# Kernel tuning notes

Measured on AMD Instinct MI355X. Metric: run time of the kernel, lower is better.

## Reference

```python
import jax, jax.numpy as jnp
import numpy as np

DIM = 192
HEADS = 4
EPS = 1e-12  # F.normalize default eps


def setup_inputs() -> dict:
    key = jax.random.key(0)
    k0, k1, k2, k3 = jax.random.split(key, 4)
    x = jax.random.normal(k0, (4, DIM, 128, 128), dtype=jnp.float32)
    # qkv 1x1 conv weight: [3*dim, dim, 1, 1] -> stored as [3*dim, dim]
    w_qkv = jax.random.normal(k1, (3 * DIM, DIM), dtype=jnp.float32) * (1.0 / np.sqrt(DIM))
    # depthwise 3x3 conv weight: [3*dim, 1, 3, 3]
    w_dw = jax.random.normal(k2, (3 * DIM, 1, 3, 3), dtype=jnp.float32) * (1.0 / 3.0)
    # project_out 1x1 conv weight: [dim, dim]
    w_proj = jax.random.normal(k3, (DIM, DIM), dtype=jnp.float32) * (1.0 / np.sqrt(DIM))
    # temperature: ones(heads,1,1), requires_grad=False in original
    temperature = jnp.ones((HEADS, 1, 1), dtype=jnp.float32)
    return {"x": x, "w_qkv": w_qkv, "w_dw": w_dw, "w_proj": w_proj,
            "temperature": temperature}


def _l2norm(t):
    # F.normalize(t, dim=-1): t / max(||t||_2, eps)
    n = jnp.sqrt(jnp.sum(t * t, axis=-1, keepdims=True))
    return t / jnp.maximum(n, EPS)


def reference(x, w_qkv, w_dw, w_proj, temperature):
    b, c, h, w = x.shape
    ch = c // HEADS  # channels per head
    # 1x1 conv (no bias) == channel GEMM
    qkv = jnp.einsum('oc,bchw->bohw', w_qkv, x)
    # depthwise 3x3 conv, padding=1, groups=3*dim
    qkv = jax.lax.conv_general_dilated(
        qkv, w_dw, window_strides=(1, 1), padding=((1, 1), (1, 1)),
        dimension_numbers=('NCHW', 'OIHW', 'NCHW'),
        feature_group_count=3 * c)
    q, k, v = jnp.split(qkv, 3, axis=1)
    # b (head ch) h w -> b head ch (h w)
    def rearr(t):
        return t.reshape(b, HEADS, ch, h * w)
    q, k, v = rearr(q), rearr(k), rearr(v)
    q = _l2norm(q)
    k = _l2norm(k)
    # channel-channel attention: [b, head, ch, ch]
    attn = jnp.einsum('bhcn,bhdn->bhcd', q, k) * temperature[None]
    attn = jax.nn.softmax(attn, axis=-1)
    out = jnp.einsum('bhcd,bhdn->bhcn', attn, v)
    out = out.reshape(b, c, h, w)
    out = jnp.einsum('oc,bchw->bohw', w_proj, out)
    return out
```

## Files before the change

### kernel.cpp

```cpp
#include <hip/hip_runtime.h>

typedef unsigned short u16;
typedef float f32x4 __attribute__((ext_vector_type(4)));
typedef __bf16 bf16x8 __attribute__((ext_vector_type(8)));
typedef unsigned short u16x8 __attribute__((ext_vector_type(8)));

#define DEV static __device__ __forceinline__

DEV u16 f2bf(float f) {
  unsigned int u = __float_as_uint(f);
  u += 0x7FFFu + ((u >> 16) & 1u);
  return (u16)(u >> 16);
}
DEV float bf2f(u16 h) { return __uint_as_float(((unsigned int)h) << 16); }
DEV u16 to_bf(float f) { return f2bf(f); }
DEV u16 to_bf(u16 h) { return h; }

DEV void gload_lds16(const void* g, void* l) {
  __builtin_amdgcn_global_load_lds(
      (__attribute__((address_space(1))) void*)(unsigned long long)g,
      (__attribute__((address_space(3))) void*)l, 16, 0, 0);
}

__global__ __launch_bounds__(256) void convert_w_kernel(
    const float* __restrict__ in, u16* __restrict__ out, int n) {
  int i = blockIdx.x * 256 + threadIdx.x;
  if (i < n) out[i] = f2bf(in[i]);
}

template <typename TIN>
__global__ __launch_bounds__(256) void transpose_kernel(
    const TIN* __restrict__ in, u16* __restrict__ out,
    size_t inBatch, size_t outBatch, int C) {
  __shared__ u16 ls[64][66];
  const int b = blockIdx.z;
  const int c0 = blockIdx.x * 64, r0 = blockIdx.y * 64;
  const TIN* ip = in + (size_t)b * inBatch;
  u16* op = out + (size_t)b * outBatch;
  const int lane = threadIdx.x & 63, w = threadIdx.x >> 6;
#pragma unroll
  for (int i = 0; i < 16; ++i) {
    const int r = i * 4 + w;
    ls[r][lane] = to_bf(ip[(size_t)(r0 + r) * C + c0 + lane]);
  }
  __syncthreads();
#pragma unroll
  for (int i = 0; i < 16; ++i) {
    const int c = i * 4 + w;
    op[(size_t)(c0 + c) * 192 + r0 + lane] = ls[lane][c];
  }
}

template <bool OUT_BF16>
__global__ __launch_bounds__(256) void gemm_bt_kernel(
    const u16* __restrict__ A, const u16* __restrict__ B, void* __restrict__ Cv,
    size_t aBatch, size_t bBatch, size_t cBatch, int ldC) {
  __shared__ __align__(16) char smem[64 * 129 * 4];
  u16* sA = (u16*)smem;
  u16* sB = (u16*)(smem + 8192);
  float* sC = (float*)smem;

  const int tid = threadIdx.x, wave = tid >> 6, lane = tid & 63;
  const int j0 = blockIdx.x * 64, m0 = blockIdx.y * 128, b = blockIdx.z;
  const u16* Ab = A + (size_t)b * aBatch + (size_t)m0 * 192;
  const u16* Bb = B + (size_t)b * bBatch + (size_t)j0 * 192;
  const int wm = wave & 1, wn = wave >> 1;
  const int l15 = lane & 15, lg = lane >> 4;

  f32x4 acc[4][2];
#pragma unroll
  for (int mi = 0; mi < 4; ++mi)
#pragma unroll
    for (int nj = 0; nj < 2; ++nj) acc[mi][nj] = (f32x4){0.f, 0.f, 0.f, 0.f};

  for (int ks = 0; ks < 6; ++ks) {
    const int k0b = ks * 64;
#pragma unroll
    for (int i = 0; i < 2; ++i) {
      const int flat = (i * 4 + wave) * 1024 + lane * 16;
      const int row = flat >> 6, colb = flat & 63;
      gload_lds16((const char*)Ab + (size_t)row * 384 + k0b + colb,
                  (char*)sA + (i * 4 + wave) * 1024);
    }
    {
      const int flat = wave * 1024 + lane * 16;
      const int row = flat >> 6, colb = flat & 63;
      gload_lds16((const char*)Bb + (size_t)row * 384 + k0b + colb,
                  (char*)sB + wave * 1024);
    }
    asm volatile("s_waitcnt vmcnt(0)" ::: "memory");
    __syncthreads();

    bf16x8 af[4], bfv[2];
#pragma unroll
    for (int mi = 0; mi < 4; ++mi)
      af[mi] = *(const bf16x8*)(sA + ((wm * 64 + mi * 16 + l15) * 32 + lg * 8));
#pragma unroll
    for (int nj = 0; nj < 2; ++nj)
      bfv[nj] = *(const bf16x8*)(sB + ((wn * 32 + nj * 16 + l15) * 32 + lg * 8));
#pragma unroll
    for (int mi = 0; mi < 4; ++mi)
#pragma unroll
      for (int nj = 0; nj < 2; ++nj)
        acc[mi][nj] = __builtin_amdgcn_mfma_f32_16x16x32_bf16(
            af[mi], bfv[nj], acc[mi][nj], 0, 0, 0);
    __syncthreads();
  }

#pragma unroll
  for (int mi = 0; mi < 4; ++mi)
#pragma unroll
    for (int nj = 0; nj < 2; ++nj)
#pragma unroll
      for (int r = 0; r < 4; ++r)
        sC[(wn * 32 + nj * 16 + l15) * 129 + (wm * 64 + mi * 16 + lg * 4 + r)] =
            acc[mi][nj][r];
  __syncthreads();
  if (OUT_BF16) {
    u16* Cb = (u16*)Cv + (size_t)b * cBatch;
#pragma unroll
    for (int i = 0; i < 32; ++i) {
      const int flat = i * 256 + tid;
      const int j = flat >> 7, m = flat & 127;
      Cb[(size_t)(j0 + j) * ldC + m0 + m] = f2bf(sC[j * 129 + m]);
    }
  } else {
    float* Cb = (float*)Cv + (size_t)b * cBatch;
#pragma unroll
    for (int i = 0; i < 32; ++i) {
      const int flat = i * 256 + tid;
      const int j = flat >> 7, m = flat & 127;
      Cb[(size_t)(j0 + j) * ldC + m0 + m] = sC[j * 129 + m];
    }
  }
}

__global__ __launch_bounds__(256) void dwconv_kernel(
    u16* __restrict__ qkv, const float* __restrict__ wdw,
    float* __restrict__ sq) {
  __shared__ u16 img[16384];
  __shared__ float red[4];
  const int o = blockIdx.x, b = blockIdx.y;
  const size_t base = ((size_t)b * 576 + o) * 16384;
  const int tid = threadIdx.x, wave = tid >> 6, lane = tid & 63;
#pragma unroll
  for (int i = 0; i < 8; ++i) {
    const int off = (i * 4 + wave) * 1024;
    gload_lds16((const char*)qkv + base * 2 + off + lane * 16, (char*)img + off);
  }
  asm volatile("s_waitcnt vmcnt(0)" ::: "memory");
  __syncthreads();
  float w[9];
#pragma unroll
  for (int j = 0; j < 9; ++j) w[j] = wdw[o * 9 + j];
  float sqacc = 0.f;
  for (int it = 0; it < 8; ++it) {
    const int chunk = it * 256 + tid;
    const int px0 = chunk * 8;
    const int y = px0 >> 7, x0 = px0 & 127;
    float acc[8];
#pragma unroll
    for (int j = 0; j < 8; ++j) acc[j] = 0.f;
#pragma unroll
    for (int dy = -1; dy <= 1; ++dy) {
      const int yy = y + dy;
      float v[10];
      if (yy >= 0 && yy <= 127) {
        const u16* rowp = img + yy * 128 + x0;
        u16x8 m = *(const u16x8*)rowp;
#pragma unroll
        for (int j = 0; j < 8; ++j) v[j + 1] = bf2f(m[j]);
        v[0] = (x0 > 0) ? bf2f(rowp[-1]) : 0.f;
        v[9] = (x0 < 120) ? bf2f(rowp[8]) : 0.f;
      } else {
#pragma unroll
        for (int j = 0; j < 10; ++j) v[j] = 0.f;
      }
      const float w0 = w[(dy + 1) * 3], w1 = w[(dy + 1) * 3 + 1],
                  w2 = w[(dy + 1) * 3 + 2];
#pragma unroll
      for (int j = 0; j < 8; ++j) acc[j] += w0 * v[j] + w1 * v[j + 1] + w2 * v[j + 2];
    }
    u16x8 ov;
#pragma unroll
    for (int j = 0; j < 8; ++j) {
      sqacc += acc[j] * acc[j];
      ov[j] = f2bf(acc[j]);
    }
    *(u16x8*)(qkv + base + px0) = ov;
  }
#pragma unroll
  for (int s = 32; s > 0; s >>= 1) sqacc += __shfl_xor(sqacc, s, 64);
  if (lane == 0) red[wave] = sqacc;
  __syncthreads();
  if (tid == 0) sq[b * 576 + o] = red[0] + red[1] + red[2] + red[3];
}

__global__ __launch_bounds__(256) void gram_kernel(
    const u16* __restrict__ qkv, float* __restrict__ partial) {
  __shared__ u16 tiles[4 * 3072];
  __shared__ float red[4 * 2304];
  const int bh = blockIdx.y, b = bh >> 2, h = bh & 3;
  const int g = blockIdx.x;
  const int wave = threadIdx.x >> 6, lane = threadIdx.x & 63;
  const int n0 = g * 1024 + wave * 256;
  const u16* qb = qkv + ((size_t)b * 576 + h * 48) * 16384;
  const u16* kb = qb + (size_t)192 * 16384;
  u16* tl = tiles + wave * 3072;
  f32x4 acc[3][3];
#pragma unroll
  for (int i = 0; i < 3; ++i)
#pragma unroll
    for (int j = 0; j < 3; ++j) acc[i][j] = (f32x4){0.f, 0.f, 0.f, 0.f};

  for (int ks = 0; ks < 8; ++ks) {
    const int nn = n0 + ks * 32;
    asm volatile("s_waitcnt lgkmcnt(0)" ::: "memory");
#pragma unroll
    for (int i = 0; i < 6; ++i) {
      const int flat = i * 1024 + lane * 16;
      const int row = flat >> 6, colb = flat & 63;
      const u16* src = (row < 48) ? (qb + (size_t)row * 16384 + nn)
                                  : (kb + (size_t)(row - 48) * 16384 + nn);
      gload_lds16((const char*)src + colb, (char*)tl + i * 1024);
    }
    asm volatile("s_waitcnt vmcnt(0)" ::: "memory");
    const int l15 = lane & 15, lg = lane >> 4;
    bf16x8 qf[3], kf[3];
#pragma unroll
    for (int f = 0; f < 3; ++f) {
      qf[f] = *(const bf16x8*)(tl + (f * 16 + l15) * 32 + lg * 8);
      kf[f] = *(const bf16x8*)(tl + (48 + f * 16 + l15) * 32 + lg * 8);
    }
#pragma unroll
    for (int i = 0; i < 3; ++i)
#pragma unroll
      for (int j = 0; j < 3; ++j)
        acc[i][j] = __builtin_amdgcn_mfma_f32_16x16x32_bf16(qf[i], kf[j],
                                                            acc[i][j], 0, 0, 0);
  }
  {
    const int l15 = lane & 15, lg = lane >> 4;
    float* rw = red + wave * 2304;
#pragma unroll
    for (int i = 0; i < 3; ++i)
#pragma unroll
      for (int j = 0; j < 3; ++j)
#pragma unroll
        for (int r = 0; r < 4; ++r)
          rw[(i * 16 + lg * 4 + r) * 48 + (j * 16 + l15)] = acc[i][j][r];
  }
  __syncthreads();
#pragma unroll
  for (int it = 0; it < 9; ++it) {
    const int p = it * 256 + threadIdx.x;
    const float s = red[p] + red[2304 + p] + red[4608 + p] + red[6912 + p];
    partial[((size_t)bh * 2304 + p) * 16 + g] = s;
  }
}

__global__ __launch_bounds__(256) void softmax_weff_kernel(
    const float* __restrict__ partial, const float* __restrict__ sq,
    const float* __restrict__ temp, const float* __restrict__ wproj,
    u16* __restrict__ weff) {
  __shared__ float G[2304];
  __shared__ float wp[192 * 49];
  __shared__ float nq[48], nk[48];
  const int bh = blockIdx.x, b = bh >> 2, h = bh & 3;
  const int tid = threadIdx.x;
#pragma unroll
  for (int it = 0; it < 36; ++it) {
    const int j = it * 256 + tid;
    const int o = j / 48, c = j - o * 48;
    wp[o * 49 + c] = wproj[o * 192 + h * 48 + c];
  }
#pragma unroll
  for (int it = 0; it < 9; ++it) {
    const int p = it * 256 + tid;
    const f32x4* pp = (const f32x4*)(partial + ((size_t)bh * 2304 + p) * 16);
    const f32x4 a = pp[0] + pp[1] + pp[2] + pp[3];
    G[p] = a.x + a.y + a.z + a.w;
  }
  if (tid < 48) {
    nq[tid] = fmaxf(sqrtf(sq[b * 576 + h * 48 + tid]), 1e-12f);
    nk[tid] = fmaxf(sqrtf(sq[b * 576 + 192 + h * 48 + tid]), 1e-12f);
  }
  __syncthreads();
  if (tid < 48) {
    const int r = tid;
    const float inq = temp[h] / nq[r];
    float L[48];
    float mx = -3.4e38f;
#pragma unroll 4
    for (int d = 0; d < 48; ++d) {
      const float v = G[r * 48 + d] * inq / nk[d];
      L[d] = v;
      mx = fmaxf(mx, v);
    }
    float s = 0.f;
#pragma unroll 4
    for (int d = 0; d < 48; ++d) {
      const float e = __expf(L[d] - mx);
      L[d] = e;
      s += e;
    }
    const float inv = 1.f / s;
#pragma unroll 4
    for (int d = 0; d < 48; ++d) G[r * 48 + d] = L[d] * inv;
  }
  __syncthreads();
  if (tid < 192) {
    const int o = tid;
    f32x4 acc[12];
#pragma unroll
    for (int dv = 0; dv < 12; ++dv) acc[dv] = (f32x4){0.f, 0.f, 0.f, 0.f};
    for (int c = 0; c < 48; ++c) {
      const float w = wp[o * 49 + c];
      const f32x4* at = (const f32x4*)(G + c * 48);
#pragma unroll
      for (int dv = 0; dv < 12; ++dv) acc[dv] += w * at[dv];
    }
    u16* op = weff + ((size_t)b * 192 + o) * 192 + h * 48;
#pragma unroll
    for (int g8 = 0; g8 < 6; ++g8) {
      u16x8 ov;
#pragma unroll
      for (int j = 0; j < 8; ++j) {
        const int d = g8 * 8 + j;
        ov[j] = f2bf(acc[d >> 2][d & 3]);
      }
      *(u16x8*)(op + g8 * 8) = ov;
    }
  }
}

extern "C" void kernel_launch(void* const* d_in, const int* in_sizes, int n_in,
                              void* d_out, int out_size, void* d_ws,
                              size_t ws_size, hipStream_t stream) {
  (void)in_sizes; (void)n_in; (void)out_size; (void)ws_size;
  const float* x      = (const float*)d_in[0];
  const float* w_qkv  = (const float*)d_in[1];
  const float* w_dw   = (const float*)d_in[2];
  const float* w_proj = (const float*)d_in[3];
  const float* temp   = (const float*)d_in[4];

  char* ws = (char*)d_ws;
  u16*   qkv     = (u16*)ws;
  u16*   vT      = (u16*)(ws + 75497472);
  float* partial = (float*)(ws + 100663296);
  float* sq      = (float*)(ws + 103022592);
  u16*   Wq      = (u16*)(ws + 103031808);
  u16*   Weff    = (u16*)(ws + 103252992);
  u16*   Xt      = (u16*)d_out;

  convert_w_kernel<<<dim3(432), 256, 0, stream>>>(w_qkv, Wq, 110592);
  transpose_kernel<float><<<dim3(256, 3, 4), 256, 0, stream>>>(
      x, Xt, (size_t)192 * 16384, (size_t)16384 * 192, 16384);
  gemm_bt_kernel<true><<<dim3(9, 128, 4), 256, 0, stream>>>(
      Xt, Wq, qkv, (size_t)16384 * 192, 0, (size_t)576 * 16384, 16384);
  dwconv_kernel<<<dim3(576, 4), 256, 0, stream>>>(qkv, w_dw, sq);
  gram_kernel<<<dim3(16, 16), 256, 0, stream>>>(qkv, partial);
  softmax_weff_kernel<<<dim3(16), 256, 0, stream>>>(partial, sq, temp, w_proj,
                                                    Weff);
  transpose_kernel<u16><<<dim3(256, 3, 4), 256, 0, stream>>>(
      qkv + (size_t)384 * 16384, vT, (size_t)576 * 16384, (size_t)16384 * 192,
      16384);
  gemm_bt_kernel<false><<<dim3(3, 128, 4), 256, 0, stream>>>(
      vT, Weff, d_out, (size_t)16384 * 192, (size_t)192 * 192,
      (size_t)192 * 16384, 16384);
}
```

Measured before the change: 160.4 us.

## Load full-K GEMM tiles once with XOR swizzle, remap blocks, vectorize transposes

The GEMM kernel now loads the whole K=192 slab of A and B into 72KB of LDS up front, using an XOR-swizzled layout to avoid bank conflicts. This removes the per-k-step loads and barriers. Blocks are launched on a 1D grid remapped across 8 XCD-style groups so neighbouring tiles share cache, and launch_bounds asks for 2 blocks per CU. Both transpose kernels switch to vectorized 16-byte global reads. The trade-off is no overlap between load and compute inside a block, plus higher LDS use that limits occupancy.

```diff
diff --git a/kernel.cpp b/kernel.cpp
--- a/kernel.cpp
+++ b/kernel.cpp
@@ -13,8 +13,6 @@
   return (u16)(u >> 16);
 }
 DEV float bf2f(u16 h) { return __uint_as_float(((unsigned int)h) << 16); }
-DEV u16 to_bf(float f) { return f2bf(f); }
-DEV u16 to_bf(u16 h) { return h; }
 
 DEV void gload_lds16(const void* g, void* l) {
   __builtin_amdgcn_global_load_lds(
@@ -28,22 +26,27 @@
   if (i < n) out[i] = f2bf(in[i]);
 }
 
-template <typename TIN>
-__global__ __launch_bounds__(256) void transpose_kernel(
-    const TIN* __restrict__ in, u16* __restrict__ out,
+__global__ __launch_bounds__(256) void transpose_f32_kernel(
+    const float* __restrict__ in, u16* __restrict__ out,
     size_t inBatch, size_t outBatch, int C) {
   __shared__ u16 ls[64][66];
   const int b = blockIdx.z;
   const int c0 = blockIdx.x * 64, r0 = blockIdx.y * 64;
-  const TIN* ip = in + (size_t)b * inBatch;
+  const float* ip = in + (size_t)b * inBatch;
   u16* op = out + (size_t)b * outBatch;
-  const int lane = threadIdx.x & 63, w = threadIdx.x >> 6;
-#pragma unroll
-  for (int i = 0; i < 16; ++i) {
-    const int r = i * 4 + w;
-    ls[r][lane] = to_bf(ip[(size_t)(r0 + r) * C + c0 + lane]);
-  }
-  __syncthreads();
+  const int t = threadIdx.x;
+  const int rr = t >> 4, cg = t & 15;
+#pragma unroll
+  for (int i = 0; i < 4; ++i) {
+    const int r = i * 16 + rr;
+    const f32x4 v = *(const f32x4*)(ip + (size_t)(r0 + r) * C + c0 + cg * 4);
+    ls[r][cg * 4 + 0] = f2bf(v.x);
+    ls[r][cg * 4 + 1] = f2bf(v.y);
+    ls[r][cg * 4 + 2] = f2bf(v.z);
+    ls[r][cg * 4 + 3] = f2bf(v.w);
+  }
+  __syncthreads();
+  const int lane = t & 63, w = t >> 6;
 #pragma unroll
   for (int i = 0; i < 16; ++i) {
     const int c = i * 4 + w;
@@ -51,21 +54,74 @@
   }
 }
 
-template <bool OUT_BF16>
-__global__ __launch_bounds__(256) void gemm_bt_kernel(
+__global__ __launch_bounds__(256) void transpose_u16_kernel(
+    const u16* __restrict__ in, u16* __restrict__ out,
+    size_t inBatch, size_t outBatch, int C) {
+  __shared__ u16 ls[64][66];
+  const int b = blockIdx.z;
+  const int c0 = blockIdx.x * 64, r0 = blockIdx.y * 64;
+  const u16* ip = in + (size_t)b * inBatch;
+  u16* op = out + (size_t)b * outBatch;
+  const int t = threadIdx.x;
+  const int rr = t >> 3, cg = t & 7;
+#pragma unroll
+  for (int i = 0; i < 2; ++i) {
+    const int r = i * 32 + rr;
+    const u16x8 v = *(const u16x8*)(ip + (size_t)(r0 + r) * C + c0 + cg * 8);
+#pragma unroll
+    for (int j = 0; j < 8; ++j) ls[r][cg * 8 + j] = v[j];
+  }
+  __syncthreads();
+  const int lane = t & 63, w = t >> 6;
+#pragma unroll
+  for (int i = 0; i < 16; ++i) {
+    const int c = i * 4 + w;
+    op[(size_t)(c0 + c) * 192 + r0 + lane] = ls[lane][c];
+  }
+}
+
+template <bool OUT_BF16, int NJ>
+__global__ __launch_bounds__(256, 2) void gemm_bt_kernel(
     const u16* __restrict__ A, const u16* __restrict__ B, void* __restrict__ Cv,
-    size_t aBatch, size_t bBatch, size_t cBatch, int ldC) {
-  __shared__ __align__(16) char smem[64 * 129 * 4];
+    size_t aBatch, size_t bBatch, size_t cBatch, int ldC, int nwg) {
+  __shared__ __align__(16) char smem[73728];
   u16* sA = (u16*)smem;
-  u16* sB = (u16*)(smem + 8192);
+  u16* sB = (u16*)(smem + 49152);
   float* sC = (float*)smem;
 
   const int tid = threadIdx.x, wave = tid >> 6, lane = tid & 63;
-  const int j0 = blockIdx.x * 64, m0 = blockIdx.y * 128, b = blockIdx.z;
-  const u16* Ab = A + (size_t)b * aBatch + (size_t)m0 * 192;
-  const u16* Bb = B + (size_t)b * bBatch + (size_t)j0 * 192;
+  const int p = blockIdx.x;
+  const int id = (p & 7) * (nwg >> 3) + (p >> 3);
+  const int j = id % NJ;
+  const int tt = id / NJ;
+  const int m0 = (tt & 127) * 128, j0 = j * 64, b = tt >> 7;
+
+  const char* Ab = (const char*)(A + (size_t)b * aBatch + (size_t)m0 * 192);
+  const char* Bb = (const char*)(B + (size_t)b * bBatch + (size_t)j0 * 192);
+
+#pragma unroll
+  for (int i = 0; i < 12; ++i) {
+    const int c = i * 4 + wave;
+    const int d = c * 1024 + lane * 16;
+    const int row = d / 384, inrow = d - row * 384;
+    gload_lds16(Ab + row * 384 + (inrow ^ ((row & 7) << 4)),
+                (char*)sA + c * 1024);
+  }
+#pragma unroll
+  for (int i = 0; i < 6; ++i) {
+    const int c = i * 4 + wave;
+    const int d = c * 1024 + lane * 16;
+    const int row = d / 384, inrow = d - row * 384;
+    gload_lds16(Bb + row * 384 + (inrow ^ ((row & 7) << 4)),
+                (char*)sB + c * 1024);
+  }
+  asm volatile("s_waitcnt vmcnt(0)" ::: "memory");
+  __syncthreads();
+
   const int wm = wave & 1, wn = wave >> 1;
   const int l15 = lane & 15, lg = lane >> 4;
+  const int swm = (l15 & 7) << 4;
+  const int rA0 = (wm * 64 + l15) * 384, rB0 = (wn * 32 + l15) * 384;
 
   f32x4 acc[4][2];
 #pragma unroll
@@ -73,39 +129,24 @@
 #pragma unroll
     for (int nj = 0; nj < 2; ++nj) acc[mi][nj] = (f32x4){0.f, 0.f, 0.f, 0.f};
 
+#pragma unroll
   for (int ks = 0; ks < 6; ++ks) {
-    const int k0b = ks * 64;
-#pragma unroll
-    for (int i = 0; i < 2; ++i) {
-      const int flat = (i * 4 + wave) * 1024 + lane * 16;
-      const int row = flat >> 6, colb = flat & 63;
-      gload_lds16((const char*)Ab + (size_t)row * 384 + k0b + colb,
-                  (char*)sA + (i * 4 + wave) * 1024);
-    }
-    {
-      const int flat = wave * 1024 + lane * 16;
-      const int row = flat >> 6, colb = flat & 63;
-      gload_lds16((const char*)Bb + (size_t)row * 384 + k0b + colb,
-                  (char*)sB + wave * 1024);
-    }
-    asm volatile("s_waitcnt vmcnt(0)" ::: "memory");
-    __syncthreads();
-
+    const int col = (ks * 64 + lg * 16) ^ swm;
     bf16x8 af[4], bfv[2];
 #pragma unroll
     for (int mi = 0; mi < 4; ++mi)
-      af[mi] = *(const bf16x8*)(sA + ((wm * 64 + mi * 16 + l15) * 32 + lg * 8));
+      af[mi] = *(const bf16x8*)((char*)sA + rA0 + mi * 16 * 384 + col);
 #pragma unroll
     for (int nj = 0; nj < 2; ++nj)
-      bfv[nj] = *(const bf16x8*)(sB + ((wn * 32 + nj * 16 + l15) * 32 + lg * 8));
+      bfv[nj] = *(const bf16x8*)((char*)sB + rB0 + nj * 16 * 384 + col);
 #pragma unroll
     for (int mi = 0; mi < 4; ++mi)
 #pragma unroll
       for (int nj = 0; nj < 2; ++nj)
         acc[mi][nj] = __builtin_amdgcn_mfma_f32_16x16x32_bf16(
             af[mi], bfv[nj], acc[mi][nj], 0, 0, 0);
-    __syncthreads();
-  }
+  }
+  __syncthreads();
 
 #pragma unroll
   for (int mi = 0; mi < 4; ++mi)
@@ -121,16 +162,16 @@
 #pragma unroll
     for (int i = 0; i < 32; ++i) {
       const int flat = i * 256 + tid;
-      const int j = flat >> 7, m = flat & 127;
-      Cb[(size_t)(j0 + j) * ldC + m0 + m] = f2bf(sC[j * 129 + m]);
+      const int jj = flat >> 7, mm = flat & 127;
+      Cb[(size_t)(j0 + jj) * ldC + m0 + mm] = f2bf(sC[jj * 129 + mm]);
     }
   } else {
     float* Cb = (float*)Cv + (size_t)b * cBatch;
 #pragma unroll
     for (int i = 0; i < 32; ++i) {
       const int flat = i * 256 + tid;
-      const int j = flat >> 7, m = flat & 127;
-      Cb[(size_t)(j0 + j) * ldC + m0 + m] = sC[j * 129 + m];
+      const int jj = flat >> 7, mm = flat & 127;
+      Cb[(size_t)(j0 + jj) * ldC + m0 + mm] = sC[jj * 129 + mm];
     }
   }
 }
@@ -354,18 +395,18 @@
   u16*   Xt      = (u16*)d_out;
 
   convert_w_kernel<<<dim3(432), 256, 0, stream>>>(w_qkv, Wq, 110592);
-  transpose_kernel<float><<<dim3(256, 3, 4), 256, 0, stream>>>(
+  transpose_f32_kernel<<<dim3(256, 3, 4), 256, 0, stream>>>(
       x, Xt, (size_t)192 * 16384, (size_t)16384 * 192, 16384);
-  gemm_bt_kernel<true><<<dim3(9, 128, 4), 256, 0, stream>>>(
-      Xt, Wq, qkv, (size_t)16384 * 192, 0, (size_t)576 * 16384, 16384);
+  gemm_bt_kernel<true, 9><<<dim3(4608), 256, 0, stream>>>(
+      Xt, Wq, qkv, (size_t)16384 * 192, 0, (size_t)576 * 16384, 16384, 4608);
   dwconv_kernel<<<dim3(576, 4), 256, 0, stream>>>(qkv, w_dw, sq);
   gram_kernel<<<dim3(16, 16), 256, 0, stream>>>(qkv, partial);
   softmax_weff_kernel<<<dim3(16), 256, 0, stream>>>(partial, sq, temp, w_proj,
                                                     Weff);
-  transpose_kernel<u16><<<dim3(256, 3, 4), 256, 0, stream>>>(
+  transpose_u16_kernel<<<dim3(256, 3, 4), 256, 0, stream>>>(
       qkv + (size_t)384 * 16384, vT, (size_t)576 * 16384, (size_t)16384 * 192,
       16384);
-  gemm_bt_kernel<false><<<dim3(3, 128, 4), 256, 0, stream>>>(
+  gemm_bt_kernel<false, 3><<<dim3(1536), 256, 0, stream>>>(
       vT, Weff, d_out, (size_t)16384 * 192, (size_t)192 * 192,
-      (size_t)192 * 16384, 16384);
-}
+      (size_t)192 * 16384, 16384, 1536);
+}
```

Result: faster. 143.0 us (-10.8%).
